# Kernel optimization log

Measured on AMD Instinct MI355X. Metric: run time of the kernel, lower is better.

The kernel has to match this reference:

```python
import jax, jax.numpy as jnp
import numpy as np

N_NODES = 100_000
N_EDGES = 1_600_000
NUM_BASIS = 10
MAX_RADIUS = 5.0
NUM_NEIGHBORS = 10.0


def _sph_harm_lmax2(u):
    # u: [E,3] unit vectors. e3nn real spherical harmonics, lmax=2,
    # normalization='component' (each l-block has per-component unit variance).
    x, y, z = u[:, 0], u[:, 1], u[:, 2]
    s3 = jnp.sqrt(3.0)
    s5 = jnp.sqrt(5.0)
    s15 = jnp.sqrt(15.0)
    return jnp.stack([
        jnp.ones_like(x),                      # l=0
        s3 * x, s3 * y, s3 * z,                # l=1
        s15 * x * z,                           # l=2
        s15 * x * y,
        s5 * (y * y - 0.5 * (x * x + z * z)),
        s15 * y * z,
        0.5 * s15 * (z * z - x * x),
    ], axis=-1)                                # [E,9]


def _soft_one_hot_smooth_finite(r):
    # e3nn soft_one_hot_linspace(r, 0, max_radius, num_basis, 'smooth_finite', cutoff=True)
    vals = jnp.linspace(0.0, MAX_RADIUS, NUM_BASIS + 2)
    step = vals[1] - vals[0]
    vals = vals[1:-1]
    d = (r[:, None] - vals[None, :]) / step    # [E,num_basis]
    inside = jnp.abs(d) < 1.0
    d2 = jnp.where(inside, d * d, 0.0)
    y = 1.14136 * jnp.exp(2.0) * jnp.exp(-1.0 / (1.0 - d2))
    return jnp.where(inside, y, 0.0)


def setup_inputs() -> dict:
    key = jax.random.key(0)
    k1, k2, k3, k4, k5, k6 = jax.random.split(key, 6)
    return {
        "pos": jax.random.normal(k1, (N_NODES, 3), dtype=jnp.float32),
        "node_feats": jax.random.normal(k2, (N_NODES, 9), dtype=jnp.float32),
        "W1": jax.random.normal(k3, (NUM_BASIS, 16), dtype=jnp.float32),
        "W2": jax.random.normal(k4, (16, 3), dtype=jnp.float32),
        "edge_src": jax.random.randint(k5, (N_EDGES,), 0, N_NODES, dtype=jnp.int32),
        "edge_dst": jax.random.randint(k6, (N_EDGES,), 0, N_NODES, dtype=jnp.int32),
    }


def reference(pos, node_feats, W1, W2, edge_src, edge_dst):
    # gather: per-edge geometry
    edge_vec = pos[edge_dst] - pos[edge_src]          # [E,3]
    r = jnp.linalg.norm(edge_vec, axis=-1)            # [E]
    u = edge_vec / (r[:, None] + 1e-12)
    sh = _sph_harm_lmax2(u)                           # [E,9]

    # radial embedding -> small MLP -> per-edge tensor-product weights (weight_numel=3)
    emb = _soft_one_hot_smooth_finite(r) * jnp.sqrt(jnp.float32(NUM_BASIS))
    h = jax.nn.relu(emb @ W1 / jnp.sqrt(jnp.float32(NUM_BASIS))) * jnp.sqrt(2.0)
    w = h @ W2 / jnp.sqrt(16.0)                       # [E,3]

    # FullyConnectedTensorProduct('1x0e+1x1o+1x2e', sh, '1x0e'), shared_weights=False
    # paths: 0e*0e->0e, 1o*1o->0e, 2e*2e->0e ; w3j(l,l,0)=I/sqrt(2l+1); fan-in 3 paths.
    x1 = node_feats[edge_src]                         # [E,9]
    path_s = x1[:, 0] * sh[:, 0]
    path_p = jnp.sum(x1[:, 1:4] * sh[:, 1:4], axis=-1) / jnp.sqrt(3.0)
    path_d = jnp.sum(x1[:, 4:9] * sh[:, 4:9], axis=-1) / jnp.sqrt(5.0)
    msg = (w[:, 0] * path_s + w[:, 1] * path_p + w[:, 2] * path_d) / jnp.sqrt(3.0)

    # scatter-aggregate messages to destination nodes
    node_out = jax.ops.segment_sum(msg, edge_dst, num_segments=N_NODES)
    node_out = node_out / jnp.sqrt(jnp.float32(NUM_NEIGHBORS))
    return node_out[:, None]                          # [N,1] scalar ('1x0e') per node
```

## Files before the change

kernel.cpp:

```cpp
#include <hip/hip_runtime.h>
#include <math.h>

#define N_NODES 100000
#define N_EDGES 1600000

#define BUCKETS 8
#define GSPLIT 32
#define BUCKET_NODES (N_NODES / BUCKETS)
#define NSEG (BUCKETS * GSPLIT)
#define CAP 8192
#define CPAD 32

__global__ __launch_bounds__(256) void pack_kernel(
    const float* __restrict__ pos,
    const float* __restrict__ feats,
    float4* __restrict__ posw,
    float4* __restrict__ featsw)
{
    const int i = blockIdx.x * blockDim.x + threadIdx.x;
    if (i >= N_NODES) return;
    const float* p = pos + 3 * i;
    const float* f = feats + 9 * i;
    posw[i]           = make_float4(p[0], p[1], p[2], f[0]);
    featsw[2 * i + 0] = make_float4(f[1], f[2], f[3], f[4]);
    featsw[2 * i + 1] = make_float4(f[5], f[6], f[7], f[8]);
}

__device__ __forceinline__ float edge_msg(
    const float4 a, const float4 b, const float4 c, const float4 pd,
    const float* __restrict__ sW1, const float* __restrict__ sW2)
{
    const float vx = pd.x - a.x;
    const float vy = pd.y - a.y;
    const float vz = pd.z - a.z;

    const float r   = sqrtf(vx * vx + vy * vy + vz * vz);
    const float inv = 1.0f / (r + 1e-12f);
    const float x = vx * inv, y = vy * inv, z = vz * inv;

    const float s3  = 1.7320508075688772f;
    const float s5  = 2.23606797749979f;
    const float s15 = 3.872983346207417f;
    const float sh1 = s3 * x;
    const float sh2 = s3 * y;
    const float sh3 = s3 * z;
    const float sh4 = s15 * x * z;
    const float sh5 = s15 * x * y;
    const float sh6 = s5 * (y * y - 0.5f * (x * x + z * z));
    const float sh7 = s15 * y * z;
    const float sh8 = 0.5f * s15 * (z * z - x * x);

    const float q = r * 2.2f;
    const int   k = (int)floorf(q);
    int   b0 = k - 1, b1 = k;
    const float d0 = q - (float)k;
    const float d1 = d0 - 1.0f;
    const float A = 8.43357307f;
    float e0 = 0.0f, e1 = 0.0f;
    if (b0 >= 0 && b0 < 10) {
        const float dd = d0 * d0;
        if (dd < 1.0f) e0 = A * expf(-1.0f / (1.0f - dd));
    }
    if (b1 >= 0 && b1 < 10) {
        const float dd = d1 * d1;
        if (dd < 1.0f) e1 = A * expf(-1.0f / (1.0f - dd));
    }
    b0 = (b0 >= 0 && b0 < 10) ? b0 : 0;
    b1 = (b1 >= 0 && b1 < 10) ? b1 : 0;

    const float* w1r0 = sW1 + b0 * 17;
    const float* w1r1 = sW1 + b1 * 17;
    float acc0 = 0.0f, acc1 = 0.0f, acc2 = 0.0f;
#pragma unroll
    for (int j = 0; j < 16; ++j) {
        const float hj = fmaxf(e0 * w1r0[j] + e1 * w1r1[j], 0.0f);
        acc0 = fmaf(hj, sW2[j * 3 + 0], acc0);
        acc1 = fmaf(hj, sW2[j * 3 + 1], acc1);
        acc2 = fmaf(hj, sW2[j * 3 + 2], acc2);
    }

    const float path_s = a.w;
    const float path_p = (b.x * sh1 + b.y * sh2 + b.z * sh3) * 0.5773502691896258f;
    const float path_d = (b.w * sh4 + c.x * sh5 + c.y * sh6
                        + c.z * sh7 + c.w * sh8) * 0.4472135954999579f;

    const float FINAL = 0.06454972243679028f;
    return (acc0 * path_s + acc1 * path_p + acc2 * path_d) * FINAL;
}

__global__ __launch_bounds__(256) void msg_part_kernel(
    const float4* __restrict__ posw,
    const float4* __restrict__ featsw,
    const float* __restrict__ W1,
    const float* __restrict__ W2,
    const int* __restrict__ edge_src,
    const int* __restrict__ edge_dst,
    int*  __restrict__ counters,
    int2* __restrict__ segs)
{
    __shared__ float sW1[10 * 17];
    __shared__ float sW2[16 * 3];
    __shared__ int cnt[BUCKETS];
    __shared__ int basesm[BUCKETS];
    const int t = threadIdx.x;
    if (t < 160) sW1[(t >> 4) * 17 + (t & 15)] = W1[t];
    if (t < 48)  sW2[t] = W2[t];
    if (t < BUCKETS) cnt[t] = 0;
    __syncthreads();

    const int e = blockIdx.x * 256 + t;
    const int s = edge_src[e];
    const int d = edge_dst[e];
    const float4 a  = posw[s];
    const float4 bb = featsw[2 * s + 0];
    const float4 cc = featsw[2 * s + 1];
    const float4 p  = posw[d];
    const float m = edge_msg(a, bb, cc, p, sW1, sW2);

    const int mybucket = d / BUCKET_NODES;
    const int local    = d - mybucket * BUCKET_NODES;
    const int rank = atomicAdd(&cnt[mybucket], 1);
    __syncthreads();

    const int g = blockIdx.x & (GSPLIT - 1);
    if (t < BUCKETS)
        basesm[t] = atomicAdd(&counters[(t * GSPLIT + g) * CPAD], cnt[t]);
    __syncthreads();

    const int slot = basesm[mybucket] + rank;
    if (slot < CAP)
        segs[(size_t)(mybucket * GSPLIT + g) * CAP + slot] =
            make_int2(local, __float_as_int(m));
}

__global__ __launch_bounds__(256) void scatter_kernel(
    const int* __restrict__ counters,
    const int2* __restrict__ segs,
    float* __restrict__ slabs)
{
    __shared__ float acc[BUCKET_NODES];
    const int seg = blockIdx.x;
    const int t = threadIdx.x;
    for (int i = t; i < BUCKET_NODES; i += 256) acc[i] = 0.0f;
    __syncthreads();

    int count = counters[seg * CPAD];
    if (count > CAP) count = CAP;
    const int2* sp = segs + (size_t)seg * CAP;
    for (int i = t; i < count; i += 256) {
        const int2 pr = sp[i];
        atomicAdd(&acc[pr.x], __int_as_float(pr.y));
    }
    __syncthreads();

    float* slab = slabs + (size_t)seg * BUCKET_NODES;
    for (int i = t; i < BUCKET_NODES; i += 256) slab[i] = acc[i];
}

__global__ __launch_bounds__(256) void reduce_kernel(
    const float* __restrict__ slabs, float* __restrict__ out)
{
    const int n = blockIdx.x * blockDim.x + threadIdx.x;
    if (n >= N_NODES) return;
    const int b = n / BUCKET_NODES;
    const int i = n - b * BUCKET_NODES;
    const float* sl = slabs + ((size_t)b * GSPLIT) * BUCKET_NODES + i;
    float sum = 0.0f;
#pragma unroll
    for (int g = 0; g < GSPLIT; ++g) sum += sl[(size_t)g * BUCKET_NODES];
    out[n] = sum;
}

__global__ __launch_bounds__(256) void edge_kernel_direct(
    const float* __restrict__ pos,
    const float* __restrict__ node_feats,
    const float* __restrict__ W1,
    const float* __restrict__ W2,
    const int*   __restrict__ edge_src,
    const int*   __restrict__ edge_dst,
    float* __restrict__ out)
{
    __shared__ float sW1[10 * 17];
    __shared__ float sW2[16 * 3];
    const int t = threadIdx.x;
    if (t < 160) sW1[(t >> 4) * 17 + (t & 15)] = W1[t];
    if (t < 48)  sW2[t] = W2[t];
    __syncthreads();

    const int e = blockIdx.x * blockDim.x + t;
    if (e >= N_EDGES) return;

    const int src = edge_src[e];
    const int dst = edge_dst[e];
    const float* ps = pos + 3 * src;
    const float* pd = pos + 3 * dst;
    const float* xf = node_feats + 9 * src;
    const float4 a = make_float4(ps[0], ps[1], ps[2], xf[0]);
    const float4 b = make_float4(xf[1], xf[2], xf[3], xf[4]);
    const float4 c = make_float4(xf[5], xf[6], xf[7], xf[8]);
    const float4 pdv = make_float4(pd[0], pd[1], pd[2], 0.0f);
    const float m = edge_msg(a, b, c, pdv, sW1, sW2);
    unsafeAtomicAdd(out + dst, m);
}

extern "C" void kernel_launch(void* const* d_in, const int* in_sizes, int n_in,
                              void* d_out, int out_size, void* d_ws, size_t ws_size,
                              hipStream_t stream) {
    const float* pos        = (const float*)d_in[0];
    const float* node_feats = (const float*)d_in[1];
    const float* W1         = (const float*)d_in[2];
    const float* W2         = (const float*)d_in[3];
    const int*   edge_src   = (const int*)d_in[4];
    const int*   edge_dst   = (const int*)d_in[5];
    float* out = (float*)d_out;

    const size_t posw_bytes   = (size_t)N_NODES * sizeof(float4);
    const size_t featsw_bytes = (size_t)N_NODES * 2 * sizeof(float4);
    const size_t cnt_bytes    = (size_t)NSEG * CPAD * sizeof(int);
    const size_t seg_bytes    = (size_t)NSEG * CAP * sizeof(int2);
    const size_t slab_bytes   = (size_t)NSEG * BUCKET_NODES * sizeof(float);
    const size_t need = posw_bytes + featsw_bytes + cnt_bytes + seg_bytes + slab_bytes;

    if (ws_size >= need) {
        char* w = (char*)d_ws;
        float4* posw   = (float4*)w;  w += posw_bytes;
        float4* featsw = (float4*)w;  w += featsw_bytes;
        int*    cnts   = (int*)w;     w += cnt_bytes;
        int2*   segs   = (int2*)w;    w += seg_bytes;
        float*  slabs  = (float*)w;

        hipMemsetAsync(cnts, 0, cnt_bytes, stream);
        pack_kernel<<<(N_NODES + 255) / 256, 256, 0, stream>>>(pos, node_feats, posw, featsw);
        msg_part_kernel<<<N_EDGES / 256, 256, 0, stream>>>(
            posw, featsw, W1, W2, edge_src, edge_dst, cnts, segs);
        scatter_kernel<<<NSEG, 256, 0, stream>>>(cnts, segs, slabs);
        reduce_kernel<<<(N_NODES + 255) / 256, 256, 0, stream>>>(slabs, out);
    } else {
        hipMemsetAsync(out, 0, N_NODES * sizeof(float), stream);
        edge_kernel_direct<<<(N_EDGES + 255) / 256, 256, 0, stream>>>(
            pos, node_feats, W1, W2, edge_src, edge_dst, out);
    }
}
```

Before: 129.1 us.

## Pack node positions and features as fp16 and fold counter reset into pack

Node positions and features are packed into half-precision vectors: a 32-byte source record plus an 8-byte destination position, replacing three float4 gathers for the source and one for the destination. This cuts the bytes moved per edge in the random-gather message kernel. The memset of the partition counters is also folded into the first block of the pack kernel, which removes one launch. In exchange, fp16 loses precision on positions and features, which can shift edge radii and basis weights and risks going outside the accuracy tolerance.

```diff
diff --git a/kernel.cpp b/kernel.cpp
--- a/kernel.cpp
+++ b/kernel.cpp
@@ -11,28 +11,45 @@
 #define CAP 8192
 #define CPAD 32
 
+typedef _Float16 half8 __attribute__((ext_vector_type(8)));
+typedef _Float16 half4 __attribute__((ext_vector_type(4)));
+
 __global__ __launch_bounds__(256) void pack_kernel(
     const float* __restrict__ pos,
     const float* __restrict__ feats,
-    float4* __restrict__ posw,
-    float4* __restrict__ featsw)
+    half8* __restrict__ srcw,
+    half4* __restrict__ posh,
+    int*   __restrict__ counters)
 {
     const int i = blockIdx.x * blockDim.x + threadIdx.x;
+    if (blockIdx.x == 0) {
+        for (int c = threadIdx.x; c < NSEG * CPAD; c += 256) counters[c] = 0;
+    }
     if (i >= N_NODES) return;
     const float* p = pos + 3 * i;
     const float* f = feats + 9 * i;
-    posw[i]           = make_float4(p[0], p[1], p[2], f[0]);
-    featsw[2 * i + 0] = make_float4(f[1], f[2], f[3], f[4]);
-    featsw[2 * i + 1] = make_float4(f[5], f[6], f[7], f[8]);
-}
-
-__device__ __forceinline__ float edge_msg(
-    const float4 a, const float4 b, const float4 c, const float4 pd,
+    half8 a, b;
+    a[0] = (_Float16)p[0]; a[1] = (_Float16)p[1]; a[2] = (_Float16)p[2];
+    a[3] = (_Float16)f[0]; a[4] = (_Float16)f[1]; a[5] = (_Float16)f[2];
+    a[6] = (_Float16)f[3]; a[7] = (_Float16)f[4];
+    b[0] = (_Float16)f[5]; b[1] = (_Float16)f[6]; b[2] = (_Float16)f[7];
+    b[3] = (_Float16)f[8]; b[4] = (_Float16)0; b[5] = (_Float16)0;
+    b[6] = (_Float16)0;    b[7] = (_Float16)0;
+    srcw[2 * i + 0] = a;
+    srcw[2 * i + 1] = b;
+    half4 q;
+    q[0] = (_Float16)p[0]; q[1] = (_Float16)p[1]; q[2] = (_Float16)p[2];
+    q[3] = (_Float16)0;
+    posh[i] = q;
+}
+
+__device__ __forceinline__ float edge_msg_h(
+    const half8 ra, const half8 rb, const half4 pd,
     const float* __restrict__ sW1, const float* __restrict__ sW2)
 {
-    const float vx = pd.x - a.x;
-    const float vy = pd.y - a.y;
-    const float vz = pd.z - a.z;
+    const float vx = (float)pd[0] - (float)ra[0];
+    const float vy = (float)pd[1] - (float)ra[1];
+    const float vz = (float)pd[2] - (float)ra[2];
 
     const float r   = sqrtf(vx * vx + vy * vy + vz * vz);
     const float inv = 1.0f / (r + 1e-12f);
@@ -79,18 +96,20 @@
         acc2 = fmaf(hj, sW2[j * 3 + 2], acc2);
     }
 
-    const float path_s = a.w;
-    const float path_p = (b.x * sh1 + b.y * sh2 + b.z * sh3) * 0.5773502691896258f;
-    const float path_d = (b.w * sh4 + c.x * sh5 + c.y * sh6
-                        + c.z * sh7 + c.w * sh8) * 0.4472135954999579f;
+    const float path_s = (float)ra[3];
+    const float path_p = ((float)ra[4] * sh1 + (float)ra[5] * sh2
+                        + (float)ra[6] * sh3) * 0.5773502691896258f;
+    const float path_d = ((float)ra[7] * sh4 + (float)rb[0] * sh5
+                        + (float)rb[1] * sh6 + (float)rb[2] * sh7
+                        + (float)rb[3] * sh8) * 0.4472135954999579f;
 
     const float FINAL = 0.06454972243679028f;
     return (acc0 * path_s + acc1 * path_p + acc2 * path_d) * FINAL;
 }
 
 __global__ __launch_bounds__(256) void msg_part_kernel(
-    const float4* __restrict__ posw,
-    const float4* __restrict__ featsw,
+    const half8* __restrict__ srcw,
+    const half4* __restrict__ posh,
     const float* __restrict__ W1,
     const float* __restrict__ W2,
     const int* __restrict__ edge_src,
@@ -111,11 +130,10 @@
     const int e = blockIdx.x * 256 + t;
     const int s = edge_src[e];
     const int d = edge_dst[e];
-    const float4 a  = posw[s];
-    const float4 bb = featsw[2 * s + 0];
-    const float4 cc = featsw[2 * s + 1];
-    const float4 p  = posw[d];
-    const float m = edge_msg(a, bb, cc, p, sW1, sW2);
+    const half8 ra = srcw[2 * s + 0];
+    const half8 rb = srcw[2 * s + 1];
+    const half4 pd = posh[d];
+    const float m = edge_msg_h(ra, rb, pd, sW1, sW2);
 
     const int mybucket = d / BUCKET_NODES;
     const int local    = d - mybucket * BUCKET_NODES;
@@ -193,13 +211,17 @@
     const int src = edge_src[e];
     const int dst = edge_dst[e];
     const float* ps = pos + 3 * src;
-    const float* pd = pos + 3 * dst;
+    const float* pdp = pos + 3 * dst;
     const float* xf = node_feats + 9 * src;
-    const float4 a = make_float4(ps[0], ps[1], ps[2], xf[0]);
-    const float4 b = make_float4(xf[1], xf[2], xf[3], xf[4]);
-    const float4 c = make_float4(xf[5], xf[6], xf[7], xf[8]);
-    const float4 pdv = make_float4(pd[0], pd[1], pd[2], 0.0f);
-    const float m = edge_msg(a, b, c, pdv, sW1, sW2);
+    half8 ra, rb; half4 pd;
+    ra[0] = (_Float16)ps[0]; ra[1] = (_Float16)ps[1]; ra[2] = (_Float16)ps[2];
+    ra[3] = (_Float16)xf[0]; ra[4] = (_Float16)xf[1]; ra[5] = (_Float16)xf[2];
+    ra[6] = (_Float16)xf[3]; ra[7] = (_Float16)xf[4];
+    rb[0] = (_Float16)xf[5]; rb[1] = (_Float16)xf[6]; rb[2] = (_Float16)xf[7];
+    rb[3] = (_Float16)xf[8]; rb[4] = rb[5] = rb[6] = rb[7] = (_Float16)0;
+    pd[0] = (_Float16)pdp[0]; pd[1] = (_Float16)pdp[1]; pd[2] = (_Float16)pdp[2];
+    pd[3] = (_Float16)0;
+    const float m = edge_msg_h(ra, rb, pd, sW1, sW2);
     unsafeAtomicAdd(out + dst, m);
 }
 
@@ -214,25 +236,25 @@
     const int*   edge_dst   = (const int*)d_in[5];
     float* out = (float*)d_out;
 
-    const size_t posw_bytes   = (size_t)N_NODES * sizeof(float4);
-    const size_t featsw_bytes = (size_t)N_NODES * 2 * sizeof(float4);
-    const size_t cnt_bytes    = (size_t)NSEG * CPAD * sizeof(int);
-    const size_t seg_bytes    = (size_t)NSEG * CAP * sizeof(int2);
-    const size_t slab_bytes   = (size_t)NSEG * BUCKET_NODES * sizeof(float);
-    const size_t need = posw_bytes + featsw_bytes + cnt_bytes + seg_bytes + slab_bytes;
+    const size_t srcw_bytes = (size_t)N_NODES * 2 * sizeof(half8);
+    const size_t posh_bytes = (size_t)N_NODES * sizeof(half4);
+    const size_t cnt_bytes  = (size_t)NSEG * CPAD * sizeof(int);
+    const size_t seg_bytes  = (size_t)NSEG * CAP * sizeof(int2);
+    const size_t slab_bytes = (size_t)NSEG * BUCKET_NODES * sizeof(float);
+    const size_t need = srcw_bytes + posh_bytes + cnt_bytes + seg_bytes + slab_bytes;
 
     if (ws_size >= need) {
         char* w = (char*)d_ws;
-        float4* posw   = (float4*)w;  w += posw_bytes;
-        float4* featsw = (float4*)w;  w += featsw_bytes;
-        int*    cnts   = (int*)w;     w += cnt_bytes;
-        int2*   segs   = (int2*)w;    w += seg_bytes;
-        float*  slabs  = (float*)w;
-
-        hipMemsetAsync(cnts, 0, cnt_bytes, stream);
-        pack_kernel<<<(N_NODES + 255) / 256, 256, 0, stream>>>(pos, node_feats, posw, featsw);
+        half8* srcw  = (half8*)w;  w += srcw_bytes;
+        half4* posh  = (half4*)w;  w += posh_bytes;
+        int*   cnts  = (int*)w;    w += cnt_bytes;
+        int2*  segs  = (int2*)w;   w += seg_bytes;
+        float* slabs = (float*)w;
+
+        pack_kernel<<<(N_NODES + 255) / 256, 256, 0, stream>>>(
+            pos, node_feats, srcw, posh, cnts);
         msg_part_kernel<<<N_EDGES / 256, 256, 0, stream>>>(
-            posw, featsw, W1, W2, edge_src, edge_dst, cnts, segs);
+            srcw, posh, W1, W2, edge_src, edge_dst, cnts, segs);
         scatter_kernel<<<NSEG, 256, 0, stream>>>(cnts, segs, slabs);
         reduce_kernel<<<(N_NODES + 255) / 256, 256, 0, stream>>>(slabs, out);
     } else {
```

Result: faster. 122.2 us (-5.3%).
